# Kernel tuning notes

Hardware: AMD Instinct MI355X
Metric: run time of the kernel (lower is better)

Reference implementation:

```python
import jax, jax.numpy as jnp
import numpy as np

BUCKET = 64      # bucket_size
N_HASHES = 8
HEADS = 8
EMB = 256
DH = EMB // HEADS  # 32, per-head dim
SELF_ATTN_VAL = -5e4  # TOKEN_SELF_ATTN_VALUE in reformer-pytorch


def haar_dwt2_per(x):
    # one-level 2D haar DWT, periodization mode. x: [B,C,H,W] (H,W even)
    B, C, H, W = x.shape
    x = x.reshape(B, C, H // 2, 2, W // 2, 2)
    a = x[:, :, :, 0, :, 0]
    b = x[:, :, :, 0, :, 1]
    c = x[:, :, :, 1, :, 0]
    d = x[:, :, :, 1, :, 1]
    ll = (a + b + c + d) * 0.5
    lh = (a - b + c - d) * 0.5  # high-pass along W
    hl = (a + b - c - d) * 0.5  # high-pass along H
    hh = (a - b - c + d) * 0.5
    return ll, lh, hl, hh


def maxpool_3s2p1(x):
    # MaxPool2d(kernel=3, stride=2, padding=1)
    return jax.lax.reduce_window(x, -jnp.inf, jax.lax.max,
                                 (1, 1, 3, 3), (1, 1, 2, 2),
                                 ((0, 0), (0, 0), (1, 1), (1, 1)))


def _look_one_back(a):
    # concat each chunk with the previous chunk (wrap-around), along axis 2
    prev = jnp.concatenate([a[:, -1:], a[:, :-1]], axis=1)
    return jnp.concatenate([a, prev], axis=2)


def lsh_attention(qk, v, rotations):
    # qk, v: [bh, t, d]; rotations: [d, n_hashes, n_buckets//2]
    bh, t, d = qk.shape
    n_buckets = t // BUCKET
    # --- hash ---
    rotated = jnp.einsum('btf,fhi->bhti', qk, rotations)        # [bh,nh,t,nb/2]
    rotated = jnp.concatenate([rotated, -rotated], axis=-1)     # [bh,nh,t,nb]
    buckets = jnp.argmax(rotated, axis=-1)                      # [bh,nh,t]
    offsets = (jnp.arange(N_HASHES) * n_buckets)[None, :, None]
    buckets = (buckets + offsets).reshape(bh, -1)               # [bh, nh*t]
    # --- sort tokens by bucket ---
    ticker = jnp.arange(N_HASHES * t)
    bat = t * buckets + (ticker % t)[None, :]
    sticker = jnp.argsort(bat, axis=-1)                         # stable sort
    undo = jnp.argsort(sticker, axis=-1)
    st = sticker % t
    sqk = jnp.take_along_axis(qk, st[..., None], axis=1)
    sv = jnp.take_along_axis(v, st[..., None], axis=1)
    nc = N_HASHES * n_buckets
    bq_t = st.reshape(bh, nc, BUCKET)
    bqk = sqk.reshape(bh, nc, BUCKET, d)
    bv = sv.reshape(bh, nc, BUCKET, d)
    bq = bqk
    norm = jnp.linalg.norm(bqk, axis=-1, keepdims=True)
    bk = bqk / jnp.maximum(norm, 1e-6)                          # make_unit_length
    bk = _look_one_back(bk)
    bv = _look_one_back(bv)
    bkv_t = _look_one_back(bq_t[..., None])[..., 0]
    # --- bucketed attention ---
    dots = jnp.einsum('bnie,bnje->bnij', bq, bk) * (d ** -0.5)  # [bh,nc,64,128]
    self_mask = bq_t[:, :, :, None] == bkv_t[:, :, None, :]
    dots = jnp.where(self_mask, SELF_ATTN_VAL, dots)
    lse = jax.scipy.special.logsumexp(dots, axis=-1, keepdims=True)
    probs = jnp.exp(dots - lse)
    bo = jnp.einsum('bnij,bnje->bnie', probs, bv)
    so = bo.reshape(bh, -1, d)
    slog = lse.reshape(bh, -1)
    # --- unsort and combine hash rounds ---
    o = jnp.take_along_axis(so, undo[..., None], axis=1).reshape(bh, N_HASHES, t, d)
    logits = jnp.take_along_axis(slog, undo, axis=1).reshape(bh, N_HASHES, t, 1)
    w = jnp.exp(logits - jax.scipy.special.logsumexp(logits, axis=1, keepdims=True))
    return jnp.sum(o * w, axis=1)                               # [bh, t, d]


def setup_inputs() -> dict:
    key = jax.random.key(0)
    ks = jax.random.split(key, 6)
    B, C, H, W = 16, 128, 32, 32
    scale = 1.0 / np.sqrt(EMB)
    return {
        'x': jax.random.normal(ks[0], (B, C, H, W), dtype=jnp.float32),
        'w_qk': jax.random.normal(ks[1], (EMB, EMB), dtype=jnp.float32) * scale,
        'w_v': jax.random.normal(ks[2], (EMB, EMB), dtype=jnp.float32) * scale,
        'w_out': jax.random.normal(ks[3], (EMB, EMB), dtype=jnp.float32) * scale,
        'b_out': jnp.zeros((EMB,), dtype=jnp.float32),
        'rotations': jax.random.normal(ks[4], (DH, N_HASHES, 5), dtype=jnp.float32),
    }


def reference(x, w_qk, w_v, w_out, b_out, rotations):
    B = x.shape[0]
    x_spatial = maxpool_3s2p1(x)                      # [B,C,16,16]
    ll, lh, hl, hh = haar_dwt2_per(x)                 # each [B,C,16,16]
    xc = jnp.concatenate([x_spatial, ll, lh, hl, hh], axis=1)  # [B,5C,16,16]
    _, N, Hh, Ww = xc.shape
    tokens = xc.reshape(B, N, Hh * Ww)                # [B, 640, 256]
    qk = tokens @ w_qk
    v = tokens @ w_v
    qkh = qk.reshape(B, N, HEADS, DH).transpose(0, 2, 1, 3).reshape(B * HEADS, N, DH)
    vh = v.reshape(B, N, HEADS, DH).transpose(0, 2, 1, 3).reshape(B * HEADS, N, DH)
    o = lsh_attention(qkh, vh, rotations)
    o = o.reshape(B, HEADS, N, DH).transpose(0, 2, 1, 3).reshape(B, N, EMB)
    out = o @ w_out + b_out
    return out.reshape(B, N, Hh, Ww)
```

## Files before the change

kernel.cpp:

```cpp
#include <hip/hip_runtime.h>
#include <math.h>

#define B_     16
#define CIN_   128
#define NTOK_  640
#define PSP_   256
#define EMB_   256
#define HEADS_ 8
#define DH_    32
#define BH_    128
#define NH_    8
#define NBK_   10
#define NC_    80
#define TOTROWS_ 10240
#define SORTLEN_ 5120
#define VSTRIDE 136
#define OCSTR  264

typedef __attribute__((ext_vector_type(8))) short short8;
typedef __attribute__((ext_vector_type(4))) short short4v;
typedef __attribute__((ext_vector_type(4))) float f32x4;

__device__ __forceinline__ unsigned bf16r(float f) {
  return (__float_as_uint(f) + 0x8000u) >> 16;
}

__global__ __launch_bounds__(256) void k_tokens(const float* __restrict__ x,
                                                float* __restrict__ tok,
                                                const float* __restrict__ wv,
                                                const float* __restrict__ wo,
                                                unsigned short* __restrict__ wtv,
                                                unsigned short* __restrict__ wto) {
  if (blockIdx.x < 256) {
    int idx = blockIdx.x * 256 + threadIdx.x;
    int n = idx >> 8, k = idx & 255;
    wtv[idx] = (unsigned short)bf16r(wv[k * 256 + n]);
    wto[idx] = (unsigned short)bf16r(wo[k * 256 + n]);
  }
  int tid = blockIdx.x * 256 + threadIdx.x;
  int p  = tid & 255;
  int bc = tid >> 8;
  int i = p >> 4, j = p & 15;
  const float* xp = x + (size_t)bc * 1024;
  int r0 = i * 2, c0 = j * 2;

  float mx = -3.4e38f;
  #pragma unroll
  for (int dr = -1; dr <= 1; dr++) {
    int r = r0 + dr;
    if (r < 0 || r >= 32) continue;
    #pragma unroll
    for (int dc = -1; dc <= 1; dc++) {
      int cc = c0 + dc;
      if (cc < 0 || cc >= 32) continue;
      mx = fmaxf(mx, xp[r * 32 + cc]);
    }
  }
  float a  = xp[r0 * 32 + c0];
  float bv = xp[r0 * 32 + c0 + 1];
  float cv = xp[(r0 + 1) * 32 + c0];
  float dv = xp[(r0 + 1) * 32 + c0 + 1];
  float ll = (a + bv + cv + dv) * 0.5f;
  float lh = (a - bv + cv - dv) * 0.5f;
  float hl = (a + bv - cv - dv) * 0.5f;
  float hh = (a - bv - cv + dv) * 0.5f;

  int b = bc >> 7, c = bc & 127;
  float* tb = tok + (size_t)b * NTOK_ * PSP_ + p;
  tb[(size_t)(c      ) * PSP_] = mx;
  tb[(size_t)(c + 128) * PSP_] = ll;
  tb[(size_t)(c + 256) * PSP_] = lh;
  tb[(size_t)(c + 384) * PSP_] = hl;
  tb[(size_t)(c + 512) * PSP_] = hh;
}

__global__ __launch_bounds__(256) void k_gemm_qv(const float* __restrict__ A,
                                                 const float* __restrict__ Wq,
                                                 const unsigned short* __restrict__ WTv,
                                                 float* __restrict__ C,
                                                 unsigned short* __restrict__ Cb,
                                                 unsigned short* __restrict__ Cv) {
  __shared__ float As[64][68];
  __shared__ float Bs[64][64];
  int tid = threadIdx.x;

  if (blockIdx.x < 640) {
    int bx = blockIdx.x;
    int row0 = (bx >> 2) * 64, col0 = (bx & 3) * 64;
    int tx = tid & 15, ty = tid >> 4;
    float acc[4][4] = {};

    int lrow = tid >> 2, lkq = tid & 3;
    int bkr = tid >> 4, bcq = tid & 15;

    for (int k0 = 0; k0 < 256; k0 += 64) {
      float4 va[4], vb4[4];
      #pragma unroll
      for (int i = 0; i < 4; i++) {
        va[i]  = *(const float4*)(&A[(size_t)(row0 + lrow) * 256 + k0 + i * 16 + 4 * lkq]);
        vb4[i] = *(const float4*)(&Wq[(size_t)(k0 + i * 16 + bkr) * 256 + col0 + 4 * bcq]);
      }
      __syncthreads();
      #pragma unroll
      for (int i = 0; i < 4; i++) {
        As[i * 16 + 4 * lkq + 0][lrow] = va[i].x;
        As[i * 16 + 4 * lkq + 1][lrow] = va[i].y;
        As[i * 16 + 4 * lkq + 2][lrow] = va[i].z;
        As[i * 16 + 4 * lkq + 3][lrow] = va[i].w;
        *(float4*)(&Bs[i * 16 + bkr][4 * bcq]) = vb4[i];
      }
      __syncthreads();
      #pragma unroll
      for (int k = 0; k < 64; k++) {
        const float4 b4 = *(const float4*)(&Bs[k][4 * tx]);
        const float4 a4 = *(const float4*)(&As[k][4 * ty]);
        float ar[4] = {a4.x, a4.y, a4.z, a4.w};
        #pragma unroll
        for (int r = 0; r < 4; r++) {
          acc[r][0] += ar[r] * b4.x; acc[r][1] += ar[r] * b4.y;
          acc[r][2] += ar[r] * b4.z; acc[r][3] += ar[r] * b4.w;
        }
      }
    }
    #pragma unroll
    for (int r = 0; r < 4; r++) {
      float4 o;
      o.x = acc[r][0]; o.y = acc[r][1]; o.z = acc[r][2]; o.w = acc[r][3];
      size_t off = (size_t)(row0 + 4 * ty + r) * 256 + col0 + 4 * tx;
      *(float4*)(&C[off]) = o;
      uint2 ub;
      ub.x = bf16r(o.x) | (bf16r(o.y) << 16);
      ub.y = bf16r(o.z) | (bf16r(o.w) << 16);
      *(uint2*)(&Cb[off]) = ub;
    }
  } else {
    int vbk = blockIdx.x - 640;
    int wid = tid >> 6, lane = tid & 63;
    int lane15 = lane & 15, quad = lane >> 4;
    int row0 = (vbk >> 1) * 64 + wid * 16;
    int col0 = (vbk & 1) * 128;

    short8 fa[8];
    const float* arow = A + (size_t)(row0 + lane15) * 256;
    #pragma unroll
    for (int kc = 0; kc < 8; kc++) {
      float4 x0 = *(const float4*)(arow + kc * 32 + quad * 8);
      float4 x1 = *(const float4*)(arow + kc * 32 + quad * 8 + 4);
      short8 f;
      f[0] = (short)bf16r(x0.x); f[1] = (short)bf16r(x0.y);
      f[2] = (short)bf16r(x0.z); f[3] = (short)bf16r(x0.w);
      f[4] = (short)bf16r(x1.x); f[5] = (short)bf16r(x1.y);
      f[6] = (short)bf16r(x1.z); f[7] = (short)bf16r(x1.w);
      fa[kc] = f;
    }
    #pragma unroll
    for (int nt = 0; nt < 8; nt++) {
      int col = col0 + nt * 16 + lane15;
      f32x4 acc = {0.f, 0.f, 0.f, 0.f};
      const unsigned short* wrow = WTv + (size_t)col * 256;
      #pragma unroll
      for (int kc = 0; kc < 8; kc++) {
        short8 fb = *(const short8*)(wrow + kc * 32 + quad * 8);
        acc = __builtin_amdgcn_mfma_f32_16x16x32_bf16(fa[kc], fb, acc, 0, 0, 0);
      }
      #pragma unroll
      for (int rg = 0; rg < 4; rg++)
        Cv[(size_t)(row0 + 4 * quad + rg) * 256 + col] = (unsigned short)bf16r(acc[rg]);
    }
  }
}

__global__ __launch_bounds__(640) void k_sort(const float* __restrict__ qkg,
                                              const float* __restrict__ rot,
                                              int* __restrict__ st) {
  int h = blockIdx.x, bh = blockIdx.y;
  int b = bh >> 3, head = bh & 7;
  __shared__ float srot[5][32];
  __shared__ int wcnt[10][10];
  __shared__ int woff[10][10];
  __shared__ int gbase[10];
  int tid = threadIdx.x, wv = tid >> 6, ln = tid & 63;

  if (tid < 160) {
    int i = tid >> 5, f = tid & 31;
    srot[i][f] = rot[f * (NH_ * 5) + h * 5 + i];
  }
  __syncthreads();

  int t = tid;
  const float* qr = qkg + ((size_t)b * NTOK_ + t) * EMB_ + head * DH_;
  float q[32];
  #pragma unroll
  for (int d4 = 0; d4 < 8; d4++) {
    float4 f = *(const float4*)(qr + d4 * 4);
    q[d4 * 4 + 0] = f.x; q[d4 * 4 + 1] = f.y; q[d4 * 4 + 2] = f.z; q[d4 * 4 + 3] = f.w;
  }
  float r[5];
  #pragma unroll
  for (int i = 0; i < 5; i++) {
    float d = 0.f;
    #pragma unroll
    for (int dd = 0; dd < 32; dd++) d += q[dd] * srot[i][dd];
    r[i] = d;
  }
  int bi = 0; float best = r[0];
  #pragma unroll
  for (int i = 1; i < 5; i++) if (r[i] > best) { best = r[i]; bi = i; }
  #pragma unroll
  for (int i = 0; i < 5; i++) if (-r[i] > best) { best = -r[i]; bi = 5 + i; }

  int myoff = 0;
  #pragma unroll
  for (int kb = 0; kb < 10; kb++) {
    unsigned long long mask = __ballot(bi == kb);
    if (ln == 0) wcnt[wv][kb] = (int)__popcll(mask);
    if (bi == kb) myoff = (int)__popcll(mask & ((1ull << ln) - 1ull));
  }
  __syncthreads();
  if (tid < 10) {
    int run = 0;
    #pragma unroll
    for (int w2 = 0; w2 < 10; w2++) { int tmp = wcnt[w2][tid]; woff[w2][tid] = run; run += tmp; }
    gbase[tid] = run;
  }
  __syncthreads();
  if (tid == 0) {
    int run = 0;
    #pragma unroll
    for (int kb = 0; kb < 10; kb++) { int tmp = gbase[kb]; gbase[kb] = run; run += tmp; }
  }
  __syncthreads();
  int rank = gbase[bi] + woff[wv][bi] + myoff;
  size_t gb = (size_t)bh * SORTLEN_ + (size_t)h * 640;
  st[gb + rank] = t;
}

__global__ __launch_bounds__(256) void k_attn(const unsigned short* __restrict__ qkb,
                                              const unsigned short* __restrict__ vb,
                                              const int* __restrict__ st,
                                              unsigned short* __restrict__ osort,
                                              float* __restrict__ lseg) {
  __shared__ __attribute__((aligned(16))) short sK[4096];
  __shared__ __attribute__((aligned(16))) short sVT[32 * VSTRIDE];
  __shared__ __attribute__((aligned(16))) short sP[2304];
  __shared__ float sM[64];
  __shared__ float sIK[128];
  __shared__ int   stkv[128];

  const float scale = 0.17677669529663687f;
  const float LOG2E = 1.4426950408889634f;
  const float K2 = scale * LOG2E;
  int c = blockIdx.x, bh = blockIdx.y;
  int b = bh >> 3, head = bh & 7;
  int lane = threadIdx.x & 63, wid = threadIdx.x >> 6;
  size_t stb = (size_t)bh * SORTLEN_;

  int kv = ((wid & 1) << 6) + lane;
  int pcv = (c + NC_ - 1) % NC_;
  int p0 = (kv < 64) ? (c * 64 + kv) : (pcv * 64 + (kv - 64));
  int t0 = st[stb + p0];

  if (wid < 2) {
    stkv[kv] = t0;
    const uint4* r0 = (const uint4*)(qkb + ((size_t)(b * NTOK_ + t0)) * EMB_ + head * DH_);
    uint4 us[4] = {r0[0], r0[1], r0[2], r0[3]};
    float n0 = 0.f;
    #pragma unroll
    for (int qq = 0; qq < 4; qq++) {
      unsigned uw[4] = {us[qq].x, us[qq].y, us[qq].z, us[qq].w};
      #pragma unroll
      for (int pp = 0; pp < 4; pp++) {
        float lo = __uint_as_float(uw[pp] << 16);
        float hi = __uint_as_float(uw[pp] & 0xFFFF0000u);
        n0 += lo * lo + hi * hi;
      }
    }
    float nrm = sqrtf(n0);
    if (kv < 64) sM[kv] = nrm * scale;
    sIK[kv] = K2 / fmaxf(nrm, 1e-6f);
    int pr = kv >> 1;
    #pragma unroll
    for (int bb = 0; bb < 4; bb++) {
      int blk = ((kv & 1) << 2) | bb;
      *(uint4*)(&sK[pr * 64 + ((blk ^ (pr & 7)) << 3)]) = us[bb];
    }
  } else {
    const uint4* r0 = (const uint4*)(vb + ((size_t)(b * NTOK_ + t0)) * EMB_ + head * DH_);
    uint4 u0 = r0[0], u1 = r0[1], u2 = r0[2], u3 = r0[3];
    unsigned uw[16] = {u0.x,u0.y,u0.z,u0.w, u1.x,u1.y,u1.z,u1.w,
                       u2.x,u2.y,u2.z,u2.w, u3.x,u3.y,u3.z,u3.w};
    #pragma unroll
    for (int f = 0; f < 32; f++) {
      unsigned s = (f & 1) ? (uw[f >> 1] >> 16) : (uw[f >> 1] & 0xFFFFu);
      sVT[f * VSTRIDE + kv] = (short)s;
    }
  }
  __syncthreads();

  int lane15 = lane & 15, quad = lane >> 4;

  short8 fall[8];
  #pragma unroll
  for (int i = 0; i < 8; i++) {
    int key = 16 * i + lane15, pr = key >> 1;
    int blk = ((key & 1) << 2) | quad;
    fall[i] = *(const short8*)(&sK[pr * 64 + ((blk ^ (pr & 7)) << 3)]);
  }
  short8 fq;
  {
    int row = 16 * wid + lane15, pr = row >> 1;
    int blk = ((row & 1) << 2) | quad;
    fq = *(const short8*)(&sK[pr * 64 + ((blk ^ (pr & 7)) << 3)]);
  }
  float mrow[4], mrow2[4]; int tqr[4];
  #pragma unroll
  for (int rg = 0; rg < 4; rg++) {
    int r = 16 * wid + 4 * quad + rg;
    mrow[rg]  = sM[r];
    mrow2[rg] = mrow[rg] * LOG2E;
    tqr[rg]   = stkv[r];
  }

  f32x4 O[2];
  float lacc[4];
  #pragma unroll
  for (int vt = 0; vt < 2; vt++) { O[vt][0]=0.f; O[vt][1]=0.f; O[vt][2]=0.f; O[vt][3]=0.f; }
  #pragma unroll
  for (int rg = 0; rg < 4; rg++) lacc[rg] = 0.f;

  #pragma unroll
  for (int s = 0; s < 4; s++) {
    f32x4 z = {0.f, 0.f, 0.f, 0.f};
    f32x4 Sv[2];
    #pragma unroll
    for (int ct = 0; ct < 2; ct++)
      Sv[ct] = __builtin_amdgcn_mfma_f32_16x16x32_bf16(fq, fall[2 * s + ct], z, 0, 0, 0);

    int kt0 = stkv[32 * s + lane15];
    int kt1 = stkv[32 * s + 16 + lane15];
    float c0 = sIK[32 * s + lane15];
    float c1 = sIK[32 * s + 16 + lane15];
    #pragma unroll
    for (int ct = 0; ct < 2; ct++) {
      int kt = ct ? kt1 : kt0;
      float cc = ct ? c1 : c0;
      #pragma unroll
      for (int rg = 0; rg < 4; rg++) {
        float e = __builtin_exp2f(__builtin_fmaf(Sv[ct][rg], cc, -mrow2[rg]));
        if (kt == tqr[rg]) e = 0.f;
        lacc[rg] += e;
        sP[(16 * wid + 4 * quad + rg) * 36 + 16 * ct + lane15] = (short)bf16r(e);
      }
    }
    short8 fv[2], fp;
    #pragma unroll
    for (int vt = 0; vt < 2; vt++)
      fv[vt] = *(const short8*)(&sVT[(16 * vt + lane15) * VSTRIDE + 32 * s + (quad << 3)]);
    {
      int off = (16 * wid + lane15) * 36 + (quad << 3);
      short4v lo = *(const short4v*)(&sP[off]);
      short4v hi = *(const short4v*)(&sP[off + 4]);
      fp = __builtin_shufflevector(lo, hi, 0, 1, 2, 3, 4, 5, 6, 7);
    }
    #pragma unroll
    for (int vt = 0; vt < 2; vt++)
      O[vt] = __builtin_amdgcn_mfma_f32_16x16x32_bf16(fp, fv[vt], O[vt], 0, 0, 0);
  }

  #pragma unroll
  for (int rg = 0; rg < 4; rg++) {
    float v = lacc[rg];
    v += __shfl_xor(v, 1); v += __shfl_xor(v, 2);
    v += __shfl_xor(v, 4); v += __shfl_xor(v, 8);
    lacc[rg] = v;
  }

  __syncthreads();

  int h = c / NBK_;
  #pragma unroll
  for (int rg = 0; rg < 4; rg++) {
    float invl = 1.f / lacc[rg];
    #pragma unroll
    for (int vt = 0; vt < 2; vt++) {
      float o = O[vt][rg] * invl;
      sP[(16 * wid + 4 * quad + rg) * 32 + 16 * vt + lane15] = (short)bf16r(o);
    }
  }
  if (lane15 == 0) {
    #pragma unroll
    for (int rg = 0; rg < 4; rg++)
      lseg[((size_t)bh * NTOK_ + tqr[rg]) * NH_ + h] = mrow[rg] + __logf(lacc[rg]);
  }
  __syncthreads();
  {
    int row = threadIdx.x >> 2, seg = threadIdx.x & 3;
    int t = stkv[row];
    uint4* dst = (uint4*)(osort + (((size_t)bh * NTOK_ + t) * NH_ + h) * 32 + seg * 8);
    *dst = ((const uint4*)sP)[threadIdx.x];
  }
}

__global__ __launch_bounds__(256) void k_combine_gemm(const unsigned short* __restrict__ osort,
                                                      const float* __restrict__ lseg,
                                                      const unsigned short* __restrict__ WT,
                                                      const float* __restrict__ bias,
                                                      float* __restrict__ C) {
  __shared__ __attribute__((aligned(16))) short sOC[32 * OCSTR];
  int bid = blockIdx.x;
  int b = bid / 20, rt = bid % 20;
  int t0 = rt * 32;
  int tid = threadIdx.x;

  {
    int tk = tid & 31, head = tid >> 5;
    int bh = b * 8 + head;
    size_t base = (size_t)bh * NTOK_ + (t0 + tk);
    float l[8];
    float4 l0 = *(const float4*)(lseg + base * 8);
    float4 l1 = *(const float4*)(lseg + base * 8 + 4);
    l[0]=l0.x; l[1]=l0.y; l[2]=l0.z; l[3]=l0.w;
    l[4]=l1.x; l[5]=l1.y; l[6]=l1.z; l[7]=l1.w;
    float m = -3.4e38f;
    #pragma unroll
    for (int h = 0; h < 8; h++) m = fmaxf(m, l[h]);
    float ssum = 0.f;
    #pragma unroll
    for (int h = 0; h < 8; h++) { l[h] = __expf(l[h] - m); ssum += l[h]; }
    float inv = 1.0f / ssum;
    float acc[32] = {};
    const uint4* orows = (const uint4*)(osort + base * 256);
    #pragma unroll
    for (int h = 0; h < 8; h++) {
      float w = l[h] * inv;
      #pragma unroll
      for (int blk = 0; blk < 4; blk++) {
        uint4 u = orows[h * 4 + blk];
        unsigned uu[4] = {u.x, u.y, u.z, u.w};
        #pragma unroll
        for (int q2 = 0; q2 < 4; q2++) {
          float lo = __uint_as_float(uu[q2] << 16);
          float hi = __uint_as_float(uu[q2] & 0xFFFF0000u);
          acc[blk * 8 + q2 * 2 + 0] += w * lo;
          acc[blk * 8 + q2 * 2 + 1] += w * hi;
        }
      }
    }
    short* dst = &sOC[tk * OCSTR + head * 32];
    #pragma unroll
    for (int q4 = 0; q4 < 4; q4++) {
      uint4 u;
      u.x = bf16r(acc[q4 * 8 + 0]) | (bf16r(acc[q4 * 8 + 1]) << 16);
      u.y = bf16r(acc[q4 * 8 + 2]) | (bf16r(acc[q4 * 8 + 3]) << 16);
      u.z = bf16r(acc[q4 * 8 + 4]) | (bf16r(acc[q4 * 8 + 5]) << 16);
      u.w = bf16r(acc[q4 * 8 + 6]) | (bf16r(acc[q4 * 8 + 7]) << 16);
      *(uint4*)(dst + q4 * 8) = u;
    }
  }
  __syncthreads();

  int wid = tid >> 6, lane = tid & 63;
  int lane15 = lane & 15, quad = lane >> 4;
  int rowt = wid & 1, colh = wid >> 1;
  int lrow0 = rowt * 16;
  int col0 = colh * 128;

  short8 fa[8];
  const short* arow = &sOC[(lrow0 + lane15) * OCSTR];
  #pragma unroll
  for (int kc = 0; kc < 8; kc++)
    fa[kc] = *(const short8*)(arow + kc * 32 + quad * 8);
  #pragma unroll
  for (int nt = 0; nt < 8; nt++) {
    int col = col0 + nt * 16 + lane15;
    f32x4 acc = {0.f, 0.f, 0.f, 0.f};
    const unsigned short* wrow = WT + (size_t)col * 256;
    #pragma unroll
    for (int kc = 0; kc < 8; kc++) {
      short8 fb = *(const short8*)(wrow + kc * 32 + quad * 8);
      acc = __builtin_amdgcn_mfma_f32_16x16x32_bf16(fa[kc], fb, acc, 0, 0, 0);
    }
    float bb = bias[col];
    #pragma unroll
    for (int rg = 0; rg < 4; rg++)
      C[(size_t)(b * NTOK_ + t0 + lrow0 + 4 * quad + rg) * 256 + col] = acc[rg] + bb;
  }
}

extern "C" void kernel_launch(void* const* d_in, const int* in_sizes, int n_in,
                              void* d_out, int out_size, void* d_ws, size_t ws_size,
                              hipStream_t stream) {
  const float* x     = (const float*)d_in[0];
  const float* w_qk  = (const float*)d_in[1];
  const float* w_v   = (const float*)d_in[2];
  const float* w_out = (const float*)d_in[3];
  const float* b_out = (const float*)d_in[4];
  const float* rot   = (const float*)d_in[5];
  float* out = (float*)d_out;

  float* tokens  = (float*)d_ws;
  float* qk      = tokens + 2621440;
  unsigned short* qkb = (unsigned short*)(qk + 2621440);
  unsigned short* vbv = qkb + 2621440;
  int*   st      = (int*)(vbv + 2621440);
  float* lse     = (float*)(st + 655360);
  unsigned short* osort = (unsigned short*)(lse + 655360);
  unsigned short* wtv = osort + 20971520;
  unsigned short* wto = wtv + 65536;

  k_tokens<<<2048, 256, 0, stream>>>(x, tokens, w_v, w_out, wtv, wto);
  k_gemm_qv<<<960, 256, 0, stream>>>(tokens, w_qk, wtv, qk, qkb, vbv);
  k_sort<<<dim3(8, 128), 640, 0, stream>>>(qk, rot, st);
  k_attn<<<dim3(80, 128), 256, 0, stream>>>(qkb, vbv, st, osort, lse);
  k_combine_gemm<<<320, 256, 0, stream>>>(osort, lse, wto, b_out, out);
}
```

Measured before the change: 217.2 us.

## Compute transposed scores in attention so P stays in registers, skipping LDS round-trip

Swaps the MFMA operand order so each lane holds scores for one query across four keys. The exponentiated probabilities can then be packed with v_cvt_pk_bf16 straight into the A-operand of the PV MFMA, with V's key ordering permuted to match, removing the per-step LDS write/read of P. Row sums now reduce across quads with two shuffles and are shared through a small LDS array. One __syncthreads is removed. This relies on the permuted sVT slot mapping lining up exactly with the register layout of the packed P.

New measurement: 209.9 us. 3.4% less time.

```diff
diff --git a/kernel.cpp b/kernel.cpp
--- a/kernel.cpp
+++ b/kernel.cpp
@@ -25,6 +25,12 @@
   return (__float_as_uint(f) + 0x8000u) >> 16;
 }
 
+__device__ __forceinline__ unsigned cvt_pk_bf16(float a, float b) {
+  unsigned r;
+  asm("v_cvt_pk_bf16_f32 %0, %1, %2" : "=v"(r) : "v"(a), "v"(b));
+  return r;
+}
+
 __global__ __launch_bounds__(256) void k_tokens(const float* __restrict__ x,
                                                 float* __restrict__ tok,
                                                 const float* __restrict__ wv,
@@ -242,9 +248,10 @@
                                               float* __restrict__ lseg) {
   __shared__ __attribute__((aligned(16))) short sK[4096];
   __shared__ __attribute__((aligned(16))) short sVT[32 * VSTRIDE];
-  __shared__ __attribute__((aligned(16))) short sP[2304];
+  __shared__ __attribute__((aligned(16))) short sP[2048];
   __shared__ float sM[64];
   __shared__ float sIK[128];
+  __shared__ float sL[64];
   __shared__ int   stkv[128];
 
   const float scale = 0.17677669529663687f;
@@ -289,10 +296,11 @@
     uint4 u0 = r0[0], u1 = r0[1], u2 = r0[2], u3 = r0[3];
     unsigned uw[16] = {u0.x,u0.y,u0.z,u0.w, u1.x,u1.y,u1.z,u1.w,
                        u2.x,u2.y,u2.z,u2.w, u3.x,u3.y,u3.z,u3.w};
+    int slot = (kv & 96) | (((kv & 15) >> 2) << 3) | (((kv >> 4) & 1) << 2) | (kv & 3);
     #pragma unroll
     for (int f = 0; f < 32; f++) {
       unsigned s = (f & 1) ? (uw[f >> 1] >> 16) : (uw[f >> 1] & 0xFFFFu);
-      sVT[f * VSTRIDE + kv] = (short)s;
+      sVT[f * VSTRIDE + slot] = (short)s;
     }
   }
   __syncthreads();
@@ -312,21 +320,15 @@
     int blk = ((row & 1) << 2) | quad;
     fq = *(const short8*)(&sK[pr * 64 + ((blk ^ (pr & 7)) << 3)]);
   }
-  float mrow[4], mrow2[4]; int tqr[4];
-  #pragma unroll
-  for (int rg = 0; rg < 4; rg++) {
-    int r = 16 * wid + 4 * quad + rg;
-    mrow[rg]  = sM[r];
-    mrow2[rg] = mrow[rg] * LOG2E;
-    tqr[rg]   = stkv[r];
-  }
+
+  int   tq  = stkv[16 * wid + lane15];
+  float mq  = sM[16 * wid + lane15];
+  float mq2 = mq * LOG2E;
 
   f32x4 O[2];
-  float lacc[4];
   #pragma unroll
   for (int vt = 0; vt < 2; vt++) { O[vt][0]=0.f; O[vt][1]=0.f; O[vt][2]=0.f; O[vt][3]=0.f; }
-  #pragma unroll
-  for (int rg = 0; rg < 4; rg++) lacc[rg] = 0.f;
+  float lacc = 0.f;
 
   #pragma unroll
   for (int s = 0; s < 4; s++) {
@@ -334,63 +336,60 @@
     f32x4 Sv[2];
     #pragma unroll
     for (int ct = 0; ct < 2; ct++)
-      Sv[ct] = __builtin_amdgcn_mfma_f32_16x16x32_bf16(fq, fall[2 * s + ct], z, 0, 0, 0);
-
-    int kt0 = stkv[32 * s + lane15];
-    int kt1 = stkv[32 * s + 16 + lane15];
-    float c0 = sIK[32 * s + lane15];
-    float c1 = sIK[32 * s + 16 + lane15];
+      Sv[ct] = __builtin_amdgcn_mfma_f32_16x16x32_bf16(fall[2 * s + ct], fq, z, 0, 0, 0);
+
+    unsigned pk[2][2];
     #pragma unroll
     for (int ct = 0; ct < 2; ct++) {
-      int kt = ct ? kt1 : kt0;
-      float cc = ct ? c1 : c0;
+      const int4   k4 = *(const int4*)(&stkv[32 * s + 16 * ct + 4 * quad]);
+      const float4 c4 = *(const float4*)(&sIK[32 * s + 16 * ct + 4 * quad]);
+      int   kk[4] = {k4.x, k4.y, k4.z, k4.w};
+      float cc[4] = {c4.x, c4.y, c4.z, c4.w};
+      float e[4];
       #pragma unroll
       for (int rg = 0; rg < 4; rg++) {
-        float e = __builtin_exp2f(__builtin_fmaf(Sv[ct][rg], cc, -mrow2[rg]));
-        if (kt == tqr[rg]) e = 0.f;
-        lacc[rg] += e;
-        sP[(16 * wid + 4 * quad + rg) * 36 + 16 * ct + lane15] = (short)bf16r(e);
-      }
-    }
-    short8 fv[2], fp;
+        float v = __builtin_exp2f(__builtin_fmaf(Sv[ct][rg], cc[rg], -mq2));
+        if (kk[rg] == tq) v = 0.f;
+        lacc += v;
+        e[rg] = v;
+      }
+      pk[ct][0] = cvt_pk_bf16(e[0], e[1]);
+      pk[ct][1] = cvt_pk_bf16(e[2], e[3]);
+    }
+    short8 fp;
+    {
+      union { unsigned u[4]; short8 v; } cv_;
+      cv_.u[0] = pk[0][0]; cv_.u[1] = pk[0][1];
+      cv_.u[2] = pk[1][0]; cv_.u[3] = pk[1][1];
+      fp = cv_.v;
+    }
+    short8 fv[2];
     #pragma unroll
     for (int vt = 0; vt < 2; vt++)
       fv[vt] = *(const short8*)(&sVT[(16 * vt + lane15) * VSTRIDE + 32 * s + (quad << 3)]);
-    {
-      int off = (16 * wid + lane15) * 36 + (quad << 3);
-      short4v lo = *(const short4v*)(&sP[off]);
-      short4v hi = *(const short4v*)(&sP[off + 4]);
-      fp = __builtin_shufflevector(lo, hi, 0, 1, 2, 3, 4, 5, 6, 7);
-    }
     #pragma unroll
     for (int vt = 0; vt < 2; vt++)
       O[vt] = __builtin_amdgcn_mfma_f32_16x16x32_bf16(fp, fv[vt], O[vt], 0, 0, 0);
   }
 
+  lacc += __shfl_xor(lacc, 16);
+  lacc += __shfl_xor(lacc, 32);
+
+  int h = c / NBK_;
+  if (lane < 16) {
+    sL[16 * wid + lane] = lacc;
+    lseg[((size_t)bh * NTOK_ + tq) * NH_ + h] = mq + __logf(lacc);
+  }
+  float4 lr = *(const float4*)(&sL[16 * wid + 4 * quad]);
+  float lrow[4] = {lr.x, lr.y, lr.z, lr.w};
   #pragma unroll
   for (int rg = 0; rg < 4; rg++) {
-    float v = lacc[rg];
-    v += __shfl_xor(v, 1); v += __shfl_xor(v, 2);
-    v += __shfl_xor(v, 4); v += __shfl_xor(v, 8);
-    lacc[rg] = v;
-  }
-
-  __syncthreads();
-
-  int h = c / NBK_;
-  #pragma unroll
-  for (int rg = 0; rg < 4; rg++) {
-    float invl = 1.f / lacc[rg];
+    float invl = 1.f / lrow[rg];
     #pragma unroll
     for (int vt = 0; vt < 2; vt++) {
       float o = O[vt][rg] * invl;
       sP[(16 * wid + 4 * quad + rg) * 32 + 16 * vt + lane15] = (short)bf16r(o);
     }
-  }
-  if (lane15 == 0) {
-    #pragma unroll
-    for (int rg = 0; rg < 4; rg++)
-      lseg[((size_t)bh * NTOK_ + tqr[rg]) * NH_ + h] = mrow[rg] + __logf(lacc[rg]);
   }
   __syncthreads();
   {
```
